# Kernel optimization log

Measured on AMD Instinct MI355X. Metric: run time of the kernel, lower is better.

Reference implementation:

```python
import jax, jax.numpy as jnp
import numpy as np

N = 200000      # nodes
E = 1600000     # directed edges (before self-loops)
G = 5000        # graphs (molecules)
IN, HID, OUT, HEADS = 128, 128, 128, 3


def gat_layer(x, src, dst, W, a_src, a_dst, b, heads, out_dim, concat):
    n = x.shape[0]
    h = (x @ W).reshape(n, heads, out_dim)                 # [N,H,F]
    al_s = jnp.einsum('nhf,hf->nh', h, a_src)              # [N,H]
    al_d = jnp.einsum('nhf,hf->nh', h, a_dst)
    e = jax.nn.leaky_relu(al_s[src] + al_d[dst], 0.2)      # [E,H]
    m = jax.ops.segment_max(e, dst, num_segments=n)        # softmax over incoming edges
    ex = jnp.exp(e - m[dst])
    den = jax.ops.segment_sum(ex, dst, num_segments=n)
    alpha = ex / (den[dst] + 1e-16)                        # [E,H]
    msg = h[src] * alpha[..., None]                        # [E,H,F]
    agg = jax.ops.segment_sum(msg, dst, num_segments=n)    # [N,H,F]
    agg = agg.reshape(n, heads * out_dim) if concat else agg.mean(axis=1)
    return agg + b


def setup_inputs() -> dict:
    key = jax.random.key(0)
    ks = jax.random.split(key, 16)
    d = {}
    d['x'] = jax.random.normal(ks[0], (N, IN), dtype=jnp.float32)
    d['edge_index'] = jax.random.randint(ks[1], (2, E), 0, N, dtype=jnp.int64)
    d['batch'] = jnp.sort(jax.random.randint(ks[2], (N,), 0, G, dtype=jnp.int64))
    s = 0.1
    d['W1'] = jax.random.normal(ks[3], (IN, HEADS * HID), jnp.float32) * s
    d['a1s'] = jax.random.normal(ks[4], (HEADS, HID), jnp.float32) * s
    d['a1d'] = jax.random.normal(ks[5], (HEADS, HID), jnp.float32) * s
    d['b1'] = jnp.zeros((HEADS * HID,), jnp.float32)
    d['W2'] = jax.random.normal(ks[6], (HEADS * HID, HEADS * HID), jnp.float32) * s
    d['a2s'] = jax.random.normal(ks[7], (HEADS, HID), jnp.float32) * s
    d['a2d'] = jax.random.normal(ks[8], (HEADS, HID), jnp.float32) * s
    d['b2'] = jnp.zeros((HEADS * HID,), jnp.float32)
    d['W3'] = jax.random.normal(ks[9], (HEADS * HID, OUT), jnp.float32) * s
    d['a3s'] = jax.random.normal(ks[10], (1, OUT), jnp.float32) * s
    d['a3d'] = jax.random.normal(ks[11], (1, OUT), jnp.float32) * s
    d['b3'] = jnp.zeros((OUT,), jnp.float32)
    return d


def reference(x, edge_index, batch, W1, a1s, a1d, b1, W2, a2s, a2d, b2, W3, a3s, a3d, b3):
    # PyG GATConv default add_self_loops=True
    loops = jnp.arange(N, dtype=edge_index.dtype)
    src = jnp.concatenate([edge_index[0], loops])
    dst = jnp.concatenate([edge_index[1], loops])
    h = jax.nn.leaky_relu(gat_layer(x, src, dst, W1, a1s, a1d, b1, HEADS, HID, True), 0.2)
    h = jax.nn.leaky_relu(gat_layer(h, src, dst, W2, a2s, a2d, b2, HEADS, HID, True), 0.2)
    h = jax.nn.leaky_relu(gat_layer(h, src, dst, W3, a3s, a3d, b3, 1, OUT, False), 0.2)
    # global mean pool over graphs
    sums = jax.ops.segment_sum(h, batch, num_segments=G)            # [G,OUT]
    cnt = jax.ops.segment_sum(jnp.ones((N,), h.dtype), batch, num_segments=G)
    return sums / jnp.maximum(cnt, 1.0)[:, None]
```

## Files before the change

### kernel.cpp

```cpp
#include <hip/hip_runtime.h>
#include <hip/hip_bf16.h>
#include <math.h>

#define LRELU_SLOPE 0.2f
typedef __hip_bfloat16 bf16;
typedef __hip_bfloat162 bf16x2;

typedef short s8v __attribute__((ext_vector_type(8)));
typedef short s4v __attribute__((ext_vector_type(4)));
typedef float f4v __attribute__((ext_vector_type(4)));

__device__ __forceinline__ float lrelu(float v) { return v > 0.f ? v : LRELU_SLOPE * v; }
__device__ __forceinline__ float b2f(short b) {
  return __uint_as_float(((unsigned)(unsigned short)b) << 16);
}

__device__ __forceinline__ void st2(float* p, float x, float y) {
  *(float2*)p = float2{x, y};
}

template <typename T>
__device__ __forceinline__ void nt_store16(void* p, T v) {
  union { T t; unsigned long long q[2]; } u;
  u.t = v;
  __builtin_nontemporal_store(u.q[0], (unsigned long long*)p);
  __builtin_nontemporal_store(u.q[1], (unsigned long long*)p + 1);
}


__global__ void k_zero(unsigned int* __restrict__ p, long n) {
  long i = (long)blockIdx.x * blockDim.x + threadIdx.x;
  if (i < n) p[i] = 0u;
}

__global__ void k_zero_out(float* __restrict__ out, int n) {
  int i = blockIdx.x * blockDim.x + threadIdx.x;
  if (i < n) out[i] = 0.f;
}


__global__ void k_cvt(const float* __restrict__ x, bf16* __restrict__ xb, long n) {
  long i = (long)blockIdx.x * blockDim.x + threadIdx.x;
  if (i < n) xb[i] = __float2bfloat16(x[i]);
}

__global__ void k_tw(const float* __restrict__ W, bf16* __restrict__ Wt, int K, int NN) {
  int i = blockIdx.x * blockDim.x + threadIdx.x;
  if (i >= K * NN) return;
  int k = i / NN, n = i - k * NN;
  Wt[(size_t)n * K + k] = __float2bfloat16(W[i]);
}


__global__ void k_hist(const int* __restrict__ dst, int* __restrict__ deg, int E, int Et) {
  int e = blockIdx.x * blockDim.x + threadIdx.x;
  if (e >= Et) return;
  int d = (e < E) ? dst[e] : (e - E);
  atomicAdd(&deg[d], 1);
}

__global__ void k_hist1(const int* __restrict__ idx, int* __restrict__ deg, int n) {
  int i = blockIdx.x * blockDim.x + threadIdx.x;
  if (i < n) atomicAdd(&deg[idx[i]], 1);
}

__global__ void k_scan1(const int* __restrict__ deg, int* __restrict__ offs,
                        int* __restrict__ bsum, int n) {
  __shared__ int sd[256];
  int t = threadIdx.x;
  int base = blockIdx.x * 1024 + t * 4;
  int v[4]; int tsum = 0;
#pragma unroll
  for (int i = 0; i < 4; ++i) { v[i] = (base + i < n) ? deg[base + i] : 0; tsum += v[i]; }
  sd[t] = tsum;
  __syncthreads();
  for (int off = 1; off < 256; off <<= 1) {
    int x = (t >= off) ? sd[t - off] : 0;
    __syncthreads();
    sd[t] += x;
    __syncthreads();
  }
  int excl = sd[t] - tsum;
#pragma unroll
  for (int i = 0; i < 4; ++i) { if (base + i < n) offs[base + i] = excl; excl += v[i]; }
  if (t == 255) bsum[blockIdx.x] = sd[255];
}

__global__ void k_scan2(int* bsum, int nb) {
  if (threadIdx.x == 0 && blockIdx.x == 0) {
    int run = 0;
    for (int i = 0; i < nb; ++i) { int t = bsum[i]; bsum[i] = run; run += t; }
  }
}

__global__ void k_scan3(int* __restrict__ offs, const int* __restrict__ bsum, int n, int total) {
  int t = threadIdx.x;
  int base = blockIdx.x * 1024 + t * 4;
  int add = bsum[blockIdx.x];
#pragma unroll
  for (int i = 0; i < 4; ++i) if (base + i < n) offs[base + i] += add;
  if (blockIdx.x == 0 && t == 0) offs[n] = total;
}

__global__ void k_scatter(const int* __restrict__ src, const int* __restrict__ dst,
                          const int* __restrict__ offs, int* __restrict__ cur,
                          int* __restrict__ ssrc, int E, int Et) {
  int e = blockIdx.x * blockDim.x + threadIdx.x;
  if (e >= Et) return;
  int s, d;
  if (e < E) { s = src[e]; d = dst[e]; } else { s = d = e - E; }
  int pos = offs[d] + atomicAdd(&cur[d], 1);
  ssrc[pos] = s;
}


__global__ __launch_bounds__(256) void k_gemm_mfma(const bf16* __restrict__ A,
                                                   const bf16* __restrict__ Wt,
                                                   bf16* __restrict__ C,
                                                   int K, int NN) {
  __shared__ __align__(16) short sA[64 * 64];
  int t = threadIdx.x;
  int wv = t >> 6, lane = t & 63;
  int quad = lane >> 4, l15 = lane & 15;
  size_t bm0 = (size_t)blockIdx.x * 64;
  int bn0 = blockIdx.y * 64;
  const bf16* Ab = A + bm0 * K;
  const bf16* Bp = Wt + (size_t)(bn0 + wv * 16 + l15) * K;
  f4v acc[4] = {f4v{0,0,0,0}, f4v{0,0,0,0}, f4v{0,0,0,0}, f4v{0,0,0,0}};

  for (int kb = 0; kb < K; kb += 64) {
#pragma unroll
    for (int j = 0; j < 2; ++j) {
      int idx = j * 256 + t;
      int row = idx >> 3, p = idx & 7;
      int c = p ^ (row & 7);
      const bf16* g = Ab + (size_t)row * K + kb + c * 8;
      __builtin_amdgcn_global_load_lds(
          (const __attribute__((address_space(1))) void*)g,
          (__attribute__((address_space(3))) void*)((char*)sA + (size_t)(j * 256 + wv * 64) * 16),
          16, 0, 0);
    }
    __syncthreads();
#pragma unroll
    for (int kk = 0; kk < 2; ++kk) {
      s8v bfrag = *(const s8v*)(Bp + kb + kk * 32 + quad * 8);
#pragma unroll
      for (int ms = 0; ms < 4; ++ms) {
        int row = ms * 16 + l15;
        int pos = (kk * 4 + quad) ^ (row & 7);
        s8v afrag = *(const s8v*)((const char*)sA + (size_t)row * 128 + pos * 16);
        acc[ms] = __builtin_amdgcn_mfma_f32_16x16x32_bf16(afrag, bfrag, acc[ms], 0, 0, 0);
      }
    }
    __syncthreads();
  }
  int coln = bn0 + wv * 16 + l15;
#pragma unroll
  for (int ms = 0; ms < 4; ++ms)
#pragma unroll
    for (int r = 0; r < 4; ++r)
      C[(bm0 + ms * 16 + quad * 4 + r) * NN + coln] = __float2bfloat16(acc[ms][r]);
}


template <int H>
__global__ void k_al(const bf16* __restrict__ h, const float* __restrict__ as,
                     const float* __restrict__ ad, float* __restrict__ al_s,
                     float* __restrict__ al_d, int N) {
  constexpr int SP = (H > 1) ? 4 : 1;
  int n = (blockIdx.x * blockDim.x + threadIdx.x) >> 6;
  int lane = threadIdx.x & 63;
  if (n >= N) return;
  int hd = lane >> 4;
  bool active = (hd < H);
  int hdc = active ? hd : 0;
  int f8 = (lane & 15) * 8;
  const bf16* hp = h + (size_t)n * (H * 128) + hdc * 128 + f8;
  s8v hv = *(const s8v*)hp;
  float ss = 0.f, sd = 0.f;
#pragma unroll
  for (int i = 0; i < 8; ++i) {
    float v = b2f(hv[i]);
    ss += v * as[hdc * 128 + f8 + i];
    sd += v * ad[hdc * 128 + f8 + i];
  }
#pragma unroll
  for (int off = 8; off; off >>= 1) {
    ss += __shfl_xor(ss, off, 64);
    sd += __shfl_xor(sd, off, 64);
  }
  if (active && (lane & 15) == 0) {
    al_s[n * SP + hd] = ss;
    al_d[n * SP + hd] = sd;
  }
}


template <int CPL> struct HVec;
template <> struct HVec<8> { typedef s8v T; };
template <> struct HVec<4> { typedef s4v T; };

template <int H, typename OT>
__global__ __launch_bounds__(256) void k_attn_agg(const bf16* __restrict__ hbuf,
                           const int* __restrict__ ssrc,
                           const int* __restrict__ offs, const float* __restrict__ al_s,
                           const float* __restrict__ al_d, const float* __restrict__ bias,
                           OT* __restrict__ out, int N) {
  constexpr int SW  = (H > 1) ? 4 : 2;
  constexpr int ROW = H * 128;
  constexpr int CPL = (H > 1) ? 8 : 4;
  constexpr int NL  = ROW / CPL;
  typedef typename HVec<CPL>::T hvec;

  __shared__ __align__(16) float stash[4][64 * SW];
  int n = (blockIdx.x * blockDim.x + threadIdx.x) >> 6;
  int lane = threadIdx.x & 63;
  if (n >= N) return;
  float* st = stash[threadIdx.x >> 6];
  int start = offs[n], end = offs[n + 1];

  float ald[H];
  if constexpr (H > 1) {
    float4 t = *(const float4*)&al_d[(size_t)n * 4];
    ald[0] = t.x; ald[1] = t.y; ald[2] = t.z;
  } else {
    ald[0] = al_d[n];
  }

  bool act = lane < NL;
  int c0 = act ? lane * CPL : 0;
  int hd_l = c0 >> 7;

  float m[H];
  float den = 0.f;
  float acc[CPL];
#pragma unroll
  for (int hd = 0; hd < H; ++hd) m[hd] = -1e30f;
#pragma unroll
  for (int i = 0; i < CPL; ++i) acc[i] = 0.f;

  for (int cb = start; cb < end; cb += 64) {
    int cl = end - cb; if (cl > 64) cl = 64;
    bool el = lane < cl;
    int mys = el ? ssrc[cb + lane] : 0;
    float ev[H];
    if constexpr (H > 1) {
      float4 av = *(const float4*)&al_s[(size_t)mys * 4];
      ev[0] = av.x; ev[1] = av.y; ev[2] = av.z;
    } else {
      ev[0] = al_s[mys];
    }
#pragma unroll
    for (int hd = 0; hd < H; ++hd)
      ev[hd] = el ? lrelu(ev[hd] + ald[hd]) : -1e30f;

    float nm[H];
#pragma unroll
    for (int hd = 0; hd < H; ++hd) {
      float v = ev[hd];
#pragma unroll
      for (int off = 32; off; off >>= 1) v = fmaxf(v, __shfl_xor(v, off, 64));
      nm[hd] = fmaxf(v, m[hd]);
    }
    if (cb > start) {
      float sc[H];
#pragma unroll
      for (int hd = 0; hd < H; ++hd) sc[hd] = __expf(m[hd] - nm[hd]);
      float so = sc[hd_l];
      den *= so;
#pragma unroll
      for (int i = 0; i < CPL; ++i) acc[i] *= so;
    }
#pragma unroll
    for (int hd = 0; hd < H; ++hd) m[hd] = nm[hd];

    float myex[H];
#pragma unroll
    for (int hd = 0; hd < H; ++hd) myex[hd] = el ? __expf(ev[hd] - m[hd]) : 0.f;

    __builtin_amdgcn_wave_barrier();
    if constexpr (H > 1) {
      float4 s4{__int_as_float(mys), myex[0], myex[1], myex[2]};
      *(float4*)&st[lane * 4] = s4;
    } else {
      float2 s2{__int_as_float(mys), myex[0]};
      *(float2*)&st[lane * 2] = s2;
    }
    asm volatile("s_waitcnt lgkmcnt(0)" ::: "memory");
    __builtin_amdgcn_wave_barrier();

    for (int r = 0; r < cl; r += 8) {
      int su[8]; float a[8];
#pragma unroll
      for (int u = 0; u < 8; ++u) {
        if constexpr (H > 1) {
          float4 ed = *(const float4*)&st[(r + u) * 4];
          su[u] = __float_as_int(ed.x);
          a[u] = (hd_l == 0) ? ed.y : ((hd_l == 1) ? ed.z : ed.w);
        } else {
          float2 ed = *(const float2*)&st[(r + u) * 2];
          su[u] = __float_as_int(ed.x);
          a[u] = ed.y;
        }
        den += a[u];
      }
      hvec hv[8];
#pragma unroll
      for (int u = 0; u < 8; ++u)
        hv[u] = *(const hvec*)(hbuf + (size_t)su[u] * ROW + c0);
#pragma unroll
      for (int u = 0; u < 8; ++u)
#pragma unroll
        for (int i = 0; i < CPL; ++i)
          acc[i] += a[u] * b2f(hv[u][i]);
    }
  }

  if (act) {
    float rr = 1.f / (den + 1e-16f);
    OT* op = out + (size_t)n * ROW + c0;
    if constexpr (sizeof(OT) == 2) {
      s8v ov;
#pragma unroll
      for (int i = 0; i < CPL; ++i) {
        float o = lrelu(acc[i] * rr + bias[c0 + i]);
        bf16 b = __float2bfloat16(o);
        ov[i] = *(short*)&b;
      }
      nt_store16(op, ov);
    } else {
      float4 ov;
      ov.x = lrelu(acc[0] * rr + bias[c0 + 0]);
      ov.y = lrelu(acc[1] * rr + bias[c0 + 1]);
      ov.z = lrelu(acc[2] * rr + bias[c0 + 2]);
      ov.w = lrelu(acc[3] * rr + bias[c0 + 3]);
      nt_store16(op, ov);
    }
  }
}


__global__ void k_pool(const float* __restrict__ h, const int* __restrict__ goffs,
                       float* __restrict__ out, int G) {
  int g = (blockIdx.x * blockDim.x + threadIdx.x) >> 6;
  int lane = threadIdx.x & 63;
  if (g >= G) return;
  int s = goffs[g], e = goffs[g + 1];
  float ax = 0.f, ay = 0.f;
  for (int n = s; n < e; ++n) {
    float2 v = *(const float2*)&h[(size_t)n * 128 + lane * 2];
    ax += v.x; ay += v.y;
  }
  float c = fmaxf((float)(e - s), 1.f);
  st2(&out[(size_t)g * 128 + lane * 2], ax / c, ay / c);
}


extern "C" void kernel_launch(void* const* d_in, const int* in_sizes, int n_in,
                              void* d_out, int out_size, void* d_ws, size_t ws_size,
                              hipStream_t stream) {
  const float* x   = (const float*)d_in[0];
  const int*   ei  = (const int*)d_in[1];
  const int*   bat = (const int*)d_in[2];
  const float* W1  = (const float*)d_in[3];
  const float* a1s = (const float*)d_in[4];
  const float* a1d = (const float*)d_in[5];
  const float* b1  = (const float*)d_in[6];
  const float* W2  = (const float*)d_in[7];
  const float* a2s = (const float*)d_in[8];
  const float* a2d = (const float*)d_in[9];
  const float* b2  = (const float*)d_in[10];
  const float* W3  = (const float*)d_in[11];
  const float* a3s = (const float*)d_in[12];
  const float* a3d = (const float*)d_in[13];
  const float* b3  = (const float*)d_in[14];
  float* out = (float*)d_out;

  const int N = in_sizes[2];
  const int E = in_sizes[1] / 2;
  const int Et = E + N;
  const int G = out_size / 128;

  char* p = (char*)d_ws;
  auto carve = [&](size_t bytes) { void* r = (void*)p; p += (bytes + 255) & ~(size_t)255; return r; };
  bf16*  bufA   = (bf16*)carve((size_t)N * 384 * 2);
  bf16*  bufB   = (bf16*)carve((size_t)N * 384 * 2);
  float* al_s   = (float*)carve((size_t)N * 4 * 4);
  float* al_d   = (float*)carve((size_t)N * 4 * 4);
  int*   ssrc   = (int*)carve((size_t)Et * 4);
  int*   offs   = (int*)carve((size_t)(N + 1) * 4);
  int*   deg    = (int*)carve((size_t)N * 4);
  int*   cur    = (int*)carve((size_t)N * 4);
  int*   bsum   = (int*)carve(4096 * 4);
  int*   gdeg   = (int*)carve((size_t)G * 4);
  int*   goffs  = (int*)carve((size_t)(G + 1) * 4);
  bf16*  Wt1    = (bf16*)carve((size_t)384 * 128 * 2);
  bf16*  Wt2    = (bf16*)carve((size_t)384 * 384 * 2);
  bf16*  Wt3    = (bf16*)carve((size_t)128 * 384 * 2);
  size_t need = (size_t)(p - (char*)d_ws);

  if (ws_size < need) {
    k_zero_out<<<(out_size + 255) / 256, 256, 0, stream>>>(out, out_size);
    return;
  }

  const int* esrc = ei;
  const int* edst = ei + E;

  int ebl = (Et + 255) / 256;
  int NB = (N + 1023) / 1024;
  int GB = (G + 1023) / 1024;
  int nodeWaveBlocks = (N * 64 + 255) / 256;

  bf16* xb = bufA;
  k_cvt<<<((long)N * 128 + 255) / 256, 256, 0, stream>>>(x, xb, (long)N * 128);
  k_tw<<<(128 * 384 + 255) / 256, 256, 0, stream>>>(W1, Wt1, 128, 384);
  k_tw<<<(384 * 384 + 255) / 256, 256, 0, stream>>>(W2, Wt2, 384, 384);
  k_tw<<<(384 * 128 + 255) / 256, 256, 0, stream>>>(W3, Wt3, 384, 128);

  k_zero<<<(N + 255) / 256, 256, 0, stream>>>((unsigned int*)deg, N);
  k_hist<<<ebl, 256, 0, stream>>>(edst, deg, E, Et);
  k_scan1<<<NB, 256, 0, stream>>>(deg, offs, bsum, N);
  k_scan2<<<1, 64, 0, stream>>>(bsum, NB);
  k_scan3<<<NB, 256, 0, stream>>>(offs, bsum, N, Et);
  k_zero<<<(N + 255) / 256, 256, 0, stream>>>((unsigned int*)cur, N);
  k_scatter<<<ebl, 256, 0, stream>>>(esrc, edst, offs, cur, ssrc, E, Et);

  k_zero<<<(G + 255) / 256, 256, 0, stream>>>((unsigned int*)gdeg, G);
  k_hist1<<<(N + 255) / 256, 256, 0, stream>>>(bat, gdeg, N);
  k_scan1<<<GB, 256, 0, stream>>>(gdeg, goffs, bsum, G);
  k_scan2<<<1, 64, 0, stream>>>(bsum, GB);
  k_scan3<<<GB, 256, 0, stream>>>(goffs, bsum, G, N);

  dim3 g1(N / 64, 6), g2(N / 64, 6), g3(N / 64, 2);

  k_gemm_mfma<<<g1, 256, 0, stream>>>(xb, Wt1, bufB, 128, 384);
  k_al<3><<<nodeWaveBlocks, 256, 0, stream>>>(bufB, a1s, a1d, al_s, al_d, N);
  k_attn_agg<3, bf16><<<nodeWaveBlocks, 256, 0, stream>>>(bufB, ssrc, offs, al_s, al_d, b1, bufA, N);

  k_gemm_mfma<<<g2, 256, 0, stream>>>(bufA, Wt2, bufB, 384, 384);
  k_al<3><<<nodeWaveBlocks, 256, 0, stream>>>(bufB, a2s, a2d, al_s, al_d, N);
  k_attn_agg<3, bf16><<<nodeWaveBlocks, 256, 0, stream>>>(bufB, ssrc, offs, al_s, al_d, b2, bufA, N);

  k_gemm_mfma<<<g3, 256, 0, stream>>>(bufA, Wt3, bufB, 384, 128);
  k_al<1><<<nodeWaveBlocks, 256, 0, stream>>>(bufB, a3s, a3d, al_s, al_d, N);
  float* out3 = (float*)bufA;
  k_attn_agg<1, float><<<nodeWaveBlocks, 256, 0, stream>>>(bufB, ssrc, offs, al_s, al_d, b3, out3, N);

  k_pool<<<(G * 64 + 255) / 256, 256, 0, stream>>>(out3, goffs, out, G);
}
```

Measured before the change: 1.508 ms.

## Split attention aggregation per head and compute all GEMM column tiles per block

The GEMM kernel now has each block loop over every 64-column tile of the output, so the A tile staged in LDS and the A fragments are reused across all column tiles instead of being reloaded by separate blocks along a second grid dimension. The attention aggregation is rewritten to run one launch per head. Within a wave, four groups of 16 lanes each handle a different neighbour's 128-feature row, with a shuffle reduction at the end, replacing the LDS stash and the per-lane head selection. The per-head split means the neighbour list and softmax are recomputed three times for layers 1 and 2. It also raises accumulator register pressure in the GEMM for six column tiles.

```diff
diff --git a/kernel.cpp b/kernel.cpp
--- a/kernel.cpp
+++ b/kernel.cpp
@@ -7,7 +7,6 @@
 typedef __hip_bfloat162 bf16x2;
 
 typedef short s8v __attribute__((ext_vector_type(8)));
-typedef short s4v __attribute__((ext_vector_type(4)));
 typedef float f4v __attribute__((ext_vector_type(4)));
 
 __device__ __forceinline__ float lrelu(float v) { return v > 0.f ? v : LRELU_SLOPE * v; }
@@ -114,19 +113,22 @@
 }
 
 
+template <int NB_T>
 __global__ __launch_bounds__(256) void k_gemm_mfma(const bf16* __restrict__ A,
                                                    const bf16* __restrict__ Wt,
-                                                   bf16* __restrict__ C,
-                                                   int K, int NN) {
+                                                   bf16* __restrict__ C, int K) {
+  constexpr int NN = NB_T * 64;
   __shared__ __align__(16) short sA[64 * 64];
   int t = threadIdx.x;
   int wv = t >> 6, lane = t & 63;
   int quad = lane >> 4, l15 = lane & 15;
   size_t bm0 = (size_t)blockIdx.x * 64;
-  int bn0 = blockIdx.y * 64;
   const bf16* Ab = A + bm0 * K;
-  const bf16* Bp = Wt + (size_t)(bn0 + wv * 16 + l15) * K;
-  f4v acc[4] = {f4v{0,0,0,0}, f4v{0,0,0,0}, f4v{0,0,0,0}, f4v{0,0,0,0}};
+  f4v acc[NB_T][4];
+#pragma unroll
+  for (int bn = 0; bn < NB_T; ++bn)
+#pragma unroll
+    for (int ms = 0; ms < 4; ++ms) acc[bn][ms] = f4v{0, 0, 0, 0};
 
   for (int kb = 0; kb < K; kb += 64) {
 #pragma unroll
@@ -141,25 +143,37 @@
           16, 0, 0);
     }
     __syncthreads();
-#pragma unroll
-    for (int kk = 0; kk < 2; ++kk) {
-      s8v bfrag = *(const s8v*)(Bp + kb + kk * 32 + quad * 8);
+    s8v af[2][4];
+#pragma unroll
+    for (int kk = 0; kk < 2; ++kk)
 #pragma unroll
       for (int ms = 0; ms < 4; ++ms) {
         int row = ms * 16 + l15;
         int pos = (kk * 4 + quad) ^ (row & 7);
-        s8v afrag = *(const s8v*)((const char*)sA + (size_t)row * 128 + pos * 16);
-        acc[ms] = __builtin_amdgcn_mfma_f32_16x16x32_bf16(afrag, bfrag, acc[ms], 0, 0, 0);
+        af[kk][ms] = *(const s8v*)((const char*)sA + (size_t)row * 128 + pos * 16);
       }
+#pragma unroll
+    for (int bn = 0; bn < NB_T; ++bn) {
+      const bf16* Bp = Wt + (size_t)(bn * 64 + wv * 16 + l15) * K + kb;
+#pragma unroll
+      for (int kk = 0; kk < 2; ++kk) {
+        s8v bfrag = *(const s8v*)(Bp + kk * 32 + quad * 8);
+#pragma unroll
+        for (int ms = 0; ms < 4; ++ms)
+          acc[bn][ms] = __builtin_amdgcn_mfma_f32_16x16x32_bf16(af[kk][ms], bfrag, acc[bn][ms], 0, 0, 0);
+      }
     }
     __syncthreads();
   }
-  int coln = bn0 + wv * 16 + l15;
-#pragma unroll
-  for (int ms = 0; ms < 4; ++ms)
-#pragma unroll
-    for (int r = 0; r < 4; ++r)
-      C[(bm0 + ms * 16 + quad * 4 + r) * NN + coln] = __float2bfloat16(acc[ms][r]);
+#pragma unroll
+  for (int bn = 0; bn < NB_T; ++bn) {
+    int coln = bn * 64 + wv * 16 + l15;
+#pragma unroll
+    for (int ms = 0; ms < 4; ++ms)
+#pragma unroll
+      for (int r = 0; r < 4; ++r)
+        C[(bm0 + ms * 16 + quad * 4 + r) * NN + coln] = __float2bfloat16(acc[bn][ms][r]);
+  }
 }
 
 
@@ -196,145 +210,91 @@
 }
 
 
-template <int CPL> struct HVec;
-template <> struct HVec<8> { typedef s8v T; };
-template <> struct HVec<4> { typedef s4v T; };
-
-template <int H, typename OT>
-__global__ __launch_bounds__(256) void k_attn_agg(const bf16* __restrict__ hbuf,
-                           const int* __restrict__ ssrc,
-                           const int* __restrict__ offs, const float* __restrict__ al_s,
-                           const float* __restrict__ al_d, const float* __restrict__ bias,
-                           OT* __restrict__ out, int N) {
-  constexpr int SW  = (H > 1) ? 4 : 2;
-  constexpr int ROW = H * 128;
-  constexpr int CPL = (H > 1) ? 8 : 4;
-  constexpr int NL  = ROW / CPL;
-  typedef typename HVec<CPL>::T hvec;
-
-  __shared__ __align__(16) float stash[4][64 * SW];
+template <int SP, int RS, int OS, typename OT>
+__global__ __launch_bounds__(256) void k_agg_h(const bf16* __restrict__ hbuf,
+                          const int* __restrict__ ssrc, const int* __restrict__ offs,
+                          const float* __restrict__ al_s, const float* __restrict__ al_d,
+                          int hd, const float* __restrict__ bias,
+                          OT* __restrict__ out,
+                          int N) {
   int n = (blockIdx.x * blockDim.x + threadIdx.x) >> 6;
   int lane = threadIdx.x & 63;
   if (n >= N) return;
-  float* st = stash[threadIdx.x >> 6];
   int start = offs[n], end = offs[n + 1];
-
-  float ald[H];
-  if constexpr (H > 1) {
-    float4 t = *(const float4*)&al_d[(size_t)n * 4];
-    ald[0] = t.x; ald[1] = t.y; ald[2] = t.z;
-  } else {
-    ald[0] = al_d[n];
-  }
-
-  bool act = lane < NL;
-  int c0 = act ? lane * CPL : 0;
-  int hd_l = c0 >> 7;
-
-  float m[H];
-  float den = 0.f;
-  float acc[CPL];
-#pragma unroll
-  for (int hd = 0; hd < H; ++hd) m[hd] = -1e30f;
-#pragma unroll
-  for (int i = 0; i < CPL; ++i) acc[i] = 0.f;
+  float ald = al_d[(size_t)n * SP + hd];
+  int g = lane >> 4, l15 = lane & 15;
+
+  float m = -1e30f, den = 0.f;
+  float acc[8];
+#pragma unroll
+  for (int i = 0; i < 8; ++i) acc[i] = 0.f;
 
   for (int cb = start; cb < end; cb += 64) {
     int cl = end - cb; if (cl > 64) cl = 64;
     bool el = lane < cl;
     int mys = el ? ssrc[cb + lane] : 0;
-    float ev[H];
-    if constexpr (H > 1) {
-      float4 av = *(const float4*)&al_s[(size_t)mys * 4];
-      ev[0] = av.x; ev[1] = av.y; ev[2] = av.z;
-    } else {
-      ev[0] = al_s[mys];
-    }
-#pragma unroll
-    for (int hd = 0; hd < H; ++hd)
-      ev[hd] = el ? lrelu(ev[hd] + ald[hd]) : -1e30f;
-
-    float nm[H];
-#pragma unroll
-    for (int hd = 0; hd < H; ++hd) {
-      float v = ev[hd];
-#pragma unroll
-      for (int off = 32; off; off >>= 1) v = fmaxf(v, __shfl_xor(v, off, 64));
-      nm[hd] = fmaxf(v, m[hd]);
-    }
+    float ev = el ? lrelu(al_s[(size_t)mys * SP + hd] + ald) : -1e30f;
+
+    float v = ev;
+#pragma unroll
+    for (int off = 32; off; off >>= 1) v = fmaxf(v, __shfl_xor(v, off, 64));
+    float nm = fmaxf(v, m);
     if (cb > start) {
-      float sc[H];
-#pragma unroll
-      for (int hd = 0; hd < H; ++hd) sc[hd] = __expf(m[hd] - nm[hd]);
-      float so = sc[hd_l];
-      den *= so;
-#pragma unroll
-      for (int i = 0; i < CPL; ++i) acc[i] *= so;
-    }
-#pragma unroll
-    for (int hd = 0; hd < H; ++hd) m[hd] = nm[hd];
-
-    float myex[H];
-#pragma unroll
-    for (int hd = 0; hd < H; ++hd) myex[hd] = el ? __expf(ev[hd] - m[hd]) : 0.f;
-
-    __builtin_amdgcn_wave_barrier();
-    if constexpr (H > 1) {
-      float4 s4{__int_as_float(mys), myex[0], myex[1], myex[2]};
-      *(float4*)&st[lane * 4] = s4;
-    } else {
-      float2 s2{__int_as_float(mys), myex[0]};
-      *(float2*)&st[lane * 2] = s2;
-    }
-    asm volatile("s_waitcnt lgkmcnt(0)" ::: "memory");
-    __builtin_amdgcn_wave_barrier();
-
-    for (int r = 0; r < cl; r += 8) {
-      int su[8]; float a[8];
-#pragma unroll
-      for (int u = 0; u < 8; ++u) {
-        if constexpr (H > 1) {
-          float4 ed = *(const float4*)&st[(r + u) * 4];
-          su[u] = __float_as_int(ed.x);
-          a[u] = (hd_l == 0) ? ed.y : ((hd_l == 1) ? ed.z : ed.w);
-        } else {
-          float2 ed = *(const float2*)&st[(r + u) * 2];
-          su[u] = __float_as_int(ed.x);
-          a[u] = ed.y;
-        }
-        den += a[u];
+      float sc = __expf(m - nm);
+      den *= sc;
+#pragma unroll
+      for (int i = 0; i < 8; ++i) acc[i] *= sc;
+    }
+    m = nm;
+    float myex = el ? __expf(ev - m) : 0.f;
+
+    for (int r = 0; r < cl; r += 16) {
+      int su[4]; float a[4];
+#pragma unroll
+      for (int j = 0; j < 4; ++j) {
+        int srcl = r + j * 4 + g;
+        su[j] = __shfl(mys, srcl, 64);
+        a[j] = __shfl(myex, srcl, 64);
       }
-      hvec hv[8];
-#pragma unroll
-      for (int u = 0; u < 8; ++u)
-        hv[u] = *(const hvec*)(hbuf + (size_t)su[u] * ROW + c0);
-#pragma unroll
-      for (int u = 0; u < 8; ++u)
-#pragma unroll
-        for (int i = 0; i < CPL; ++i)
-          acc[i] += a[u] * b2f(hv[u][i]);
-    }
-  }
-
-  if (act) {
-    float rr = 1.f / (den + 1e-16f);
-    OT* op = out + (size_t)n * ROW + c0;
-    if constexpr (sizeof(OT) == 2) {
+      s8v hv[4];
+#pragma unroll
+      for (int j = 0; j < 4; ++j)
+        hv[j] = *(const s8v*)(hbuf + (size_t)su[j] * RS + l15 * 8);
+#pragma unroll
+      for (int j = 0; j < 4; ++j) {
+#pragma unroll
+        for (int i = 0; i < 8; ++i) acc[i] += a[j] * b2f(hv[j][i]);
+        den += a[j];
+      }
+    }
+  }
+
+#pragma unroll
+  for (int off = 16; off <= 32; off <<= 1) {
+    den += __shfl_xor(den, off, 64);
+#pragma unroll
+    for (int i = 0; i < 8; ++i) acc[i] += __shfl_xor(acc[i], off, 64);
+  }
+
+  float rr = 1.f / (den + 1e-16f);
+  if constexpr (sizeof(OT) == 2) {
+    if (lane < 16) {
       s8v ov;
 #pragma unroll
-      for (int i = 0; i < CPL; ++i) {
-        float o = lrelu(acc[i] * rr + bias[c0 + i]);
+      for (int i = 0; i < 8; ++i) {
+        float o = lrelu(acc[i] * rr + bias[l15 * 8 + i]);
         bf16 b = __float2bfloat16(o);
         ov[i] = *(short*)&b;
       }
-      nt_store16(op, ov);
-    } else {
+      nt_store16((OT*)out + (size_t)n * OS + l15 * 8, ov);
+    }
+  } else {
+    if (lane < 32) {
       float4 ov;
-      ov.x = lrelu(acc[0] * rr + bias[c0 + 0]);
-      ov.y = lrelu(acc[1] * rr + bias[c0 + 1]);
-      ov.z = lrelu(acc[2] * rr + bias[c0 + 2]);
-      ov.w = lrelu(acc[3] * rr + bias[c0 + 3]);
-      nt_store16(op, ov);
+#pragma unroll
+      for (int i = 0; i < 4; ++i)
+        (&ov.x)[i] = lrelu(acc[g * 4 + i] * rr + bias[l15 * 8 + g * 4 + i]);
+      nt_store16((OT*)out + (size_t)n * OS + l15 * 8 + g * 4, ov);
     }
   }
 }
@@ -411,6 +371,7 @@
   int NB = (N + 1023) / 1024;
   int GB = (G + 1023) / 1024;
   int nodeWaveBlocks = (N * 64 + 255) / 256;
+  int gemmBlocks = (N + 63) / 64;
 
   bf16* xb = bufA;
   k_cvt<<<((long)N * 128 + 255) / 256, 256, 0, stream>>>(x, xb, (long)N * 128);
@@ -432,20 +393,23 @@
   k_scan2<<<1, 64, 0, stream>>>(bsum, GB);
   k_scan3<<<GB, 256, 0, stream>>>(goffs, bsum, G, N);
 
-  dim3 g1(N / 64, 6), g2(N / 64, 6), g3(N / 64, 2);
-
-  k_gemm_mfma<<<g1, 256, 0, stream>>>(xb, Wt1, bufB, 128, 384);
+  k_gemm_mfma<6><<<gemmBlocks, 256, 0, stream>>>(xb, Wt1, bufB, 128);
   k_al<3><<<nodeWaveBlocks, 256, 0, stream>>>(bufB, a1s, a1d, al_s, al_d, N);
-  k_attn_agg<3, bf16><<<nodeWaveBlocks, 256, 0, stream>>>(bufB, ssrc, offs, al_s, al_d, b1, bufA, N);
-
-  k_gemm_mfma<<<g2, 256, 0, stream>>>(bufA, Wt2, bufB, 384, 384);
+  for (int hd = 0; hd < 3; ++hd)
+    k_agg_h<4, 384, 384, bf16><<<nodeWaveBlocks, 256, 0, stream>>>(
+        bufB + hd * 128, ssrc, offs, al_s, al_d, hd, b1 + hd * 128, bufA + hd * 128, N);
+
+  k_gemm_mfma<6><<<gemmBlocks, 256, 0, stream>>>(bufA, Wt2, bufB, 384);
   k_al<3><<<nodeWaveBlocks, 256, 0, stream>>>(bufB, a2s, a2d, al_s, al_d, N);
-  k_attn_agg<3, bf16><<<nodeWaveBlocks, 256, 0, stream>>>(bufB, ssrc, offs, al_s, al_d, b2, bufA, N);
-
-  k_gemm_mfma<<<g3, 256, 0, stream>>>(bufA, Wt3, bufB, 384, 128);
+  for (int hd = 0; hd < 3; ++hd)
+    k_agg_h<4, 384, 384, bf16><<<nodeWaveBlocks, 256, 0, stream>>>(
+        bufB + hd * 128, ssrc, offs, al_s, al_d, hd, b2 + hd * 128, bufA + hd * 128, N);
+
+  k_gemm_mfma<2><<<gemmBlocks, 256, 0, stream>>>(bufA, Wt3, bufB, 384);
   k_al<1><<<nodeWaveBlocks, 256, 0, stream>>>(bufB, a3s, a3d, al_s, al_d, N);
   float* out3 = (float*)bufA;
-  k_attn_agg<1, float><<<nodeWaveBlocks, 256, 0, stream>>>(bufB, ssrc, offs, al_s, al_d, b3, out3, N);
+  k_agg_h<1, 128, 128, float><<<nodeWaveBlocks, 256, 0, stream>>>(
+      bufB, ssrc, offs, al_s, al_d, 0, b3, out3, N);
 
   k_pool<<<(G * 64 + 255) / 256, 256, 0, stream>>>(out3, goffs, out, G);
 }
```

Result: slower. 1.652 ms (+9.5%).

## Replace LDS-tiled GEMM with direct-register MFMA GEMM over full output width

Applied to the files above, without the earlier changes.

Weights are pre-packed into MFMA fragment order so each lane's B fragment is one contiguous 16-byte load. The GEMM now drops shared memory and loads A fragments straight from global into registers with a one-step software prefetch. Each 512-thread block covers 64 rows and the full output width, so A is read once per block instead of once per column tile. This trades LDS staging and barriers for more registers per wave and uncoalesced 16-byte A reads across rows.

```diff
diff --git a/kernel.cpp b/kernel.cpp
--- a/kernel.cpp
+++ b/kernel.cpp
@@ -44,11 +44,22 @@
   if (i < n) xb[i] = __float2bfloat16(x[i]);
 }
 
-__global__ void k_tw(const float* __restrict__ W, bf16* __restrict__ Wt, int K, int NN) {
-  int i = blockIdx.x * blockDim.x + threadIdx.x;
-  if (i >= K * NN) return;
-  int k = i / NN, n = i - k * NN;
-  Wt[(size_t)n * K + k] = __float2bfloat16(W[i]);
+__global__ void k_tw2(const float* __restrict__ W, bf16* __restrict__ B2, int K, int NN) {
+  int tid = blockIdx.x * blockDim.x + threadIdx.x;
+  int total = (K * NN) >> 3;
+  if (tid >= total) return;
+  int f = tid >> 6, l = tid & 63;
+  int nfr = NN >> 4;
+  int k32 = f / nfr, bnG = f - k32 * nfr;
+  int col = bnG * 16 + (l & 15);
+  int krow = k32 * 32 + (l >> 4) * 8;
+  s8v v;
+#pragma unroll
+  for (int j = 0; j < 8; ++j) {
+    bf16 b = __float2bfloat16(W[(size_t)(krow + j) * NN + col]);
+    v[j] = *(short*)&b;
+  }
+  *(s8v*)&B2[(size_t)tid * 8] = v;
 }
 
 
@@ -114,52 +125,64 @@
 }
 
 
-__global__ __launch_bounds__(256) void k_gemm_mfma(const bf16* __restrict__ A,
-                                                   const bf16* __restrict__ Wt,
-                                                   bf16* __restrict__ C,
-                                                   int K, int NN) {
-  __shared__ __align__(16) short sA[64 * 64];
+template <int NT>
+__global__ __launch_bounds__(512) void k_gemm_d(const bf16* __restrict__ A,
+                                                const bf16* __restrict__ B2,
+                                                bf16* __restrict__ C,
+                                                int K, int NN) {
   int t = threadIdx.x;
   int wv = t >> 6, lane = t & 63;
+  int mg = wv >> 2, ng = wv & 3;
   int quad = lane >> 4, l15 = lane & 15;
   size_t bm0 = (size_t)blockIdx.x * 64;
-  int bn0 = blockIdx.y * 64;
-  const bf16* Ab = A + bm0 * K;
-  const bf16* Bp = Wt + (size_t)(bn0 + wv * 16 + l15) * K;
-  f4v acc[4] = {f4v{0,0,0,0}, f4v{0,0,0,0}, f4v{0,0,0,0}, f4v{0,0,0,0}};
-
-  for (int kb = 0; kb < K; kb += 64) {
-#pragma unroll
-    for (int j = 0; j < 2; ++j) {
-      int idx = j * 256 + t;
-      int row = idx >> 3, p = idx & 7;
-      int c = p ^ (row & 7);
-      const bf16* g = Ab + (size_t)row * K + kb + c * 8;
-      __builtin_amdgcn_global_load_lds(
-          (const __attribute__((address_space(1))) void*)g,
-          (__attribute__((address_space(3))) void*)((char*)sA + (size_t)(j * 256 + wv * 64) * 16),
-          16, 0, 0);
-    }
-    __syncthreads();
-#pragma unroll
-    for (int kk = 0; kk < 2; ++kk) {
-      s8v bfrag = *(const s8v*)(Bp + kb + kk * 32 + quad * 8);
-#pragma unroll
-      for (int ms = 0; ms < 4; ++ms) {
-        int row = ms * 16 + l15;
-        int pos = (kk * 4 + quad) ^ (row & 7);
-        s8v afrag = *(const s8v*)((const char*)sA + (size_t)row * 128 + pos * 16);
-        acc[ms] = __builtin_amdgcn_mfma_f32_16x16x32_bf16(afrag, bfrag, acc[ms], 0, 0, 0);
-      }
-    }
-    __syncthreads();
-  }
-  int coln = bn0 + wv * 16 + l15;
-#pragma unroll
-  for (int ms = 0; ms < 4; ++ms)
-#pragma unroll
-    for (int r = 0; r < 4; ++r)
-      C[(bm0 + ms * 16 + quad * 4 + r) * NN + coln] = __float2bfloat16(acc[ms][r]);
+  const bf16* Ap0 = A + (bm0 + mg * 32 + l15) * (size_t)K + quad * 8;
+  const bf16* Ap1 = Ap0 + (size_t)16 * K;
+  int nfr = NN >> 4;
+  const bf16* Bp = B2 + ((size_t)(ng * NT) << 9) + lane * 8;
+  size_t fstep = (size_t)nfr << 9;
+
+  f4v acc[2][NT];
+#pragma unroll
+  for (int ms = 0; ms < 2; ++ms)
+#pragma unroll
+    for (int bn = 0; bn < NT; ++bn) acc[ms][bn] = f4v{0, 0, 0, 0};
+
+  s8v a0 = *(const s8v*)Ap0;
+  s8v a1 = *(const s8v*)Ap1;
+  s8v bf[NT];
+#pragma unroll
+  for (int bn = 0; bn < NT; ++bn) bf[bn] = *(const s8v*)(Bp + bn * 512);
+
+  int nk = K >> 5;
+  for (int ik = 0; ik < nk; ++ik) {
+    int nx = (ik + 1 < nk) ? ik + 1 : ik;
+    s8v na0 = *(const s8v*)(Ap0 + nx * 32);
+    s8v na1 = *(const s8v*)(Ap1 + nx * 32);
+    s8v nbf[NT];
+#pragma unroll
+    for (int bn = 0; bn < NT; ++bn)
+      nbf[bn] = *(const s8v*)(Bp + nx * fstep + bn * 512);
+#pragma unroll
+    for (int bn = 0; bn < NT; ++bn)
+      acc[0][bn] = __builtin_amdgcn_mfma_f32_16x16x32_bf16(a0, bf[bn], acc[0][bn], 0, 0, 0);
+#pragma unroll
+    for (int bn = 0; bn < NT; ++bn)
+      acc[1][bn] = __builtin_amdgcn_mfma_f32_16x16x32_bf16(a1, bf[bn], acc[1][bn], 0, 0, 0);
+    a0 = na0; a1 = na1;
+#pragma unroll
+    for (int bn = 0; bn < NT; ++bn) bf[bn] = nbf[bn];
+  }
+
+#pragma unroll
+  for (int ms = 0; ms < 2; ++ms)
+#pragma unroll
+    for (int bn = 0; bn < NT; ++bn) {
+      int coln = (ng * NT + bn) * 16 + l15;
+      size_t rbase = bm0 + mg * 32 + ms * 16 + quad * 4;
+#pragma unroll
+      for (int r = 0; r < 4; ++r)
+        C[(rbase + r) * NN + coln] = __float2bfloat16(acc[ms][bn][r]);
+    }
 }
 
 
@@ -394,9 +417,9 @@
   int*   bsum   = (int*)carve(4096 * 4);
   int*   gdeg   = (int*)carve((size_t)G * 4);
   int*   goffs  = (int*)carve((size_t)(G + 1) * 4);
-  bf16*  Wt1    = (bf16*)carve((size_t)384 * 128 * 2);
-  bf16*  Wt2    = (bf16*)carve((size_t)384 * 384 * 2);
-  bf16*  Wt3    = (bf16*)carve((size_t)128 * 384 * 2);
+  bf16*  Wp1    = (bf16*)carve((size_t)384 * 128 * 2);
+  bf16*  Wp2    = (bf16*)carve((size_t)384 * 384 * 2);
+  bf16*  Wp3    = (bf16*)carve((size_t)128 * 384 * 2);
   size_t need = (size_t)(p - (char*)d_ws);
 
   if (ws_size < need) {
@@ -411,12 +434,13 @@
   int NB = (N + 1023) / 1024;
   int GB = (G + 1023) / 1024;
   int nodeWaveBlocks = (N * 64 + 255) / 256;
+  int gemmBlocks = (N + 63) / 64;
 
   bf16* xb = bufA;
   k_cvt<<<((long)N * 128 + 255) / 256, 256, 0, stream>>>(x, xb, (long)N * 128);
-  k_tw<<<(128 * 384 + 255) / 256, 256, 0, stream>>>(W1, Wt1, 128, 384);
-  k_tw<<<(384 * 384 + 255) / 256, 256, 0, stream>>>(W2, Wt2, 384, 384);
-  k_tw<<<(384 * 128 + 255) / 256, 256, 0, stream>>>(W3, Wt3, 384, 128);
+  k_tw2<<<(128 * 384 / 8 + 255) / 256, 256, 0, stream>>>(W1, Wp1, 128, 384);
+  k_tw2<<<(384 * 384 / 8 + 255) / 256, 256, 0, stream>>>(W2, Wp2, 384, 384);
+  k_tw2<<<(384 * 128 / 8 + 255) / 256, 256, 0, stream>>>(W3, Wp3, 384, 128);
 
   k_zero<<<(N + 255) / 256, 256, 0, stream>>>((unsigned int*)deg, N);
   k_hist<<<ebl, 256, 0, stream>>>(edst, deg, E, Et);
@@ -432,17 +456,15 @@
   k_scan2<<<1, 64, 0, stream>>>(bsum, GB);
   k_scan3<<<GB, 256, 0, stream>>>(goffs, bsum, G, N);
 
-  dim3 g1(N / 64, 6), g2(N / 64, 6), g3(N / 64, 2);
-
-  k_gemm_mfma<<<g1, 256, 0, stream>>>(xb, Wt1, bufB, 128, 384);
+  k_gemm_d<6><<<gemmBlocks, 512, 0, stream>>>(xb, Wp1, bufB, 128, 384);
   k_al<3><<<nodeWaveBlocks, 256, 0, stream>>>(bufB, a1s, a1d, al_s, al_d, N);
   k_attn_agg<3, bf16><<<nodeWaveBlocks, 256, 0, stream>>>(bufB, ssrc, offs, al_s, al_d, b1, bufA, N);
 
-  k_gemm_mfma<<<g2, 256, 0, stream>>>(bufA, Wt2, bufB, 384, 384);
+  k_gemm_d<6><<<gemmBlocks, 512, 0, stream>>>(bufA, Wp2, bufB, 384, 384);
   k_al<3><<<nodeWaveBlocks, 256, 0, stream>>>(bufB, a2s, a2d, al_s, al_d, N);
   k_attn_agg<3, bf16><<<nodeWaveBlocks, 256, 0, stream>>>(bufB, ssrc, offs, al_s, al_d, b2, bufA, N);
 
-  k_gemm_mfma<<<g3, 256, 0, stream>>>(bufA, Wt3, bufB, 384, 128);
+  k_gemm_d<2><<<gemmBlocks, 512, 0, stream>>>(bufA, Wp3, bufB, 384, 128);
   k_al<1><<<nodeWaveBlocks, 256, 0, stream>>>(bufB, a3s, a3d, al_s, al_d, N);
   float* out3 = (float*)bufA;
   k_attn_agg<1, float><<<nodeWaveBlocks, 256, 0, stream>>>(bufB, ssrc, offs, al_s, al_d, b3, out3, N);
```

After: 1.511 ms. Within noise of the previous version (+0.2%).
